# Optimization experiments

Measured on AMD Instinct MI355X. Metric: run time of the kernel, lower is better.

Reference implementation:

```python
import jax, jax.numpy as jnp
import numpy as np

N_NODES = 50000
N_EDGES = 800000
IN_F = 32
HID = 64
N_LAYERS = 3
BN_EPS = 1e-5


def setup_inputs() -> dict:
    key = jax.random.key(0)
    ks = jax.random.split(key, 8)
    x = jax.random.normal(ks[0], (N_NODES, IN_F), dtype=jnp.float32)
    edge_index = jax.random.randint(ks[1], (2, N_EDGES), 0, N_NODES, dtype=jnp.int64)
    W_embed = jax.random.normal(ks[2], (IN_F, HID), dtype=jnp.float32) / np.sqrt(IN_F)
    b_embed = jnp.zeros((HID,), dtype=jnp.float32)
    W_convs = jax.random.normal(ks[3], (N_LAYERS, HID, HID), dtype=jnp.float32) / np.sqrt(HID)
    b_convs = jnp.zeros((N_LAYERS, HID), dtype=jnp.float32)
    bn_gamma = jnp.ones((HID,), dtype=jnp.float32)
    bn_beta = jnp.zeros((HID,), dtype=jnp.float32)
    return {"x": x, "edge_index": edge_index, "W_embed": W_embed, "b_embed": b_embed,
            "W_convs": W_convs, "b_convs": b_convs, "bn_gamma": bn_gamma, "bn_beta": bn_beta}


def _gcn_norm(edge_index, n_nodes):
    # PyG GCNConv: add self-loops, symmetric normalization deg^-1/2 * deg^-1/2
    loops = jnp.arange(n_nodes, dtype=edge_index.dtype)
    src = jnp.concatenate([edge_index[0], loops])
    dst = jnp.concatenate([edge_index[1], loops])
    deg = jax.ops.segment_sum(jnp.ones_like(dst, dtype=jnp.float32), dst, num_segments=n_nodes)
    dinv = jax.lax.rsqrt(jnp.maximum(deg, 1.0))
    norm = dinv[src] * dinv[dst]  # [E+N]
    return src, dst, norm


def reference(x, edge_index, W_embed, b_embed, W_convs, b_convs, bn_gamma, bn_beta):
    n = x.shape[0]
    src, dst, norm = _gcn_norm(edge_index, n)

    h = jax.nn.relu(x @ W_embed + b_embed)  # [N, HID]
    for l in range(N_LAYERS):
        res = h
        # GCNConv: linear transform, then normalized neighbor aggregation
        t = h @ W_convs[l] + b_convs[l]
        msg = t[src] * norm[:, None]                           # [E+N, HID]
        agg = jax.ops.segment_sum(msg, dst, num_segments=n)    # [N, HID]
        # BatchNorm1d (training-mode batch stats), shared across layers
        mu = jnp.mean(agg, axis=0)
        var = jnp.var(agg, axis=0)
        bn = (agg - mu) * jax.lax.rsqrt(var + BN_EPS) * bn_gamma + bn_beta
        h = jax.nn.relu(bn) + res
    return h
```

## Files before the change

### kernel.cpp

```cpp
#include <hip/hip_runtime.h>

#define IN_F 32
#define HID 64
#define N_LAYERS 3
#define BN_EPS 1e-5f
#define NPLANE 4
#define PF 16

__device__ __forceinline__ unsigned short f2bf(float x) {
    unsigned u = __float_as_uint(x);
    u += 0x7fffu + ((u >> 16) & 1u);
    return (unsigned short)(u >> 16);
}
__device__ __forceinline__ float bflo(unsigned v) { return __uint_as_float(v << 16); }
__device__ __forceinline__ float bfhi(unsigned v) { return __uint_as_float(v & 0xffff0000u); }

__global__ __launch_bounds__(256) void k_zero(int* cnt, int* cursor, float* statsAll, int n) {
    int i = blockIdx.x * blockDim.x + threadIdx.x;
    if (i < n) cnt[i] = 0;
    if (i == 0) *cursor = 0;
    if (i < 2 * HID * N_LAYERS) statsAll[i] = 0.0f;
}

__global__ __launch_bounds__(256) void k_hist_rank(const int* __restrict__ dst, int* cnt,
                                                   unsigned short* __restrict__ rank, int e) {
    int i = blockIdx.x * blockDim.x + threadIdx.x;
    if (i >= e) return;
    int r = atomicAdd(&cnt[dst[i]], 1);
    rank[i] = (unsigned short)r;
}

__global__ __launch_bounds__(256) void k_assign(const int* __restrict__ cnt, int* rowbeg,
                                                float* dinv, int* cursor, int n) {
    int i = blockIdx.x * blockDim.x + threadIdx.x;
    int lane = threadIdx.x & 63;
    int c = (i < n) ? cnt[i] : 0;
    int s = c;
#pragma unroll
    for (int off = 1; off < 64; off <<= 1) {
        int t = __shfl_up(s, off, 64);
        if (lane >= off) s += t;
    }
    int total = __shfl(s, 63, 64);
    int base = 0;
    if (lane == 63) base = atomicAdd(cursor, total);
    base = __shfl(base, 63, 64);
    if (i < n) {
        rowbeg[i] = base + s - c;
        dinv[i] = rsqrtf((float)(c + 1));
    }
}

__global__ __launch_bounds__(256) void k_fill(const int* __restrict__ src,
                                              const int* __restrict__ dst,
                                              const int* __restrict__ rowbeg,
                                              const unsigned short* __restrict__ rank,
                                              unsigned short* __restrict__ csr_src, int e) {
    int i = blockIdx.x * blockDim.x + threadIdx.x;
    if (i >= e) return;
    int pos = rowbeg[dst[i]] + (int)rank[i];
    csr_src[pos] = (unsigned short)src[i];
}

__global__ __launch_bounds__(256, 4) void k_embed_conv(const float* __restrict__ x,
                                                       const float* __restrict__ We,
                                                       const float* __restrict__ be,
                                                       const float* __restrict__ Wc,
                                                       const float* __restrict__ bc,
                                                       const float* __restrict__ dinv,
                                                       float* __restrict__ h,
                                                       unsigned short* __restrict__ t2b, int n) {
    __shared__ float shx[4][IN_F];
    __shared__ float shh[4][HID];
    int f = threadIdx.x & 63;
    int wv = threadIdx.x >> 6;
    int plane = f >> 4, fin = f & 15;

    float we[IN_F];
#pragma unroll
    for (int k = 0; k < IN_F; ++k) we[k] = We[k * HID + f];
    float wc[HID];
#pragma unroll
    for (int k = 0; k < HID; ++k) wc[k] = Wc[k * HID + f];
    float bef = be[f], bcf = bc[f];

    int nw = gridDim.x * 4;
    for (int node = blockIdx.x * 4 + wv; node < n; node += nw) {
        if (f < IN_F) shx[wv][f] = x[(size_t)node * IN_F + f];
        float acc = bef;
#pragma unroll
        for (int k4 = 0; k4 < IN_F / 4; ++k4) {
            float4 xq = ((const float4*)shx[wv])[k4];
            acc = fmaf(xq.x, we[k4 * 4 + 0], acc);
            acc = fmaf(xq.y, we[k4 * 4 + 1], acc);
            acc = fmaf(xq.z, we[k4 * 4 + 2], acc);
            acc = fmaf(xq.w, we[k4 * 4 + 3], acc);
        }
        float hv = fmaxf(acc, 0.0f);
        h[(size_t)node * HID + f] = hv;
        shh[wv][f] = hv;
        float acc2 = bcf;
#pragma unroll
        for (int k4 = 0; k4 < HID / 4; ++k4) {
            float4 hq = ((const float4*)shh[wv])[k4];
            acc2 = fmaf(hq.x, wc[k4 * 4 + 0], acc2);
            acc2 = fmaf(hq.y, wc[k4 * 4 + 1], acc2);
            acc2 = fmaf(hq.z, wc[k4 * 4 + 2], acc2);
            acc2 = fmaf(hq.w, wc[k4 * 4 + 3], acc2);
        }
        t2b[(size_t)plane * n * PF + (size_t)node * PF + fin] = f2bf(acc2 * dinv[node]);
    }
}

__global__ __launch_bounds__(256, 4) void k_bn_conv(const float* __restrict__ agg,
                                                    const float* __restrict__ stats,
                                                    const float* __restrict__ gamma,
                                                    const float* __restrict__ beta,
                                                    const float* __restrict__ W,
                                                    const float* __restrict__ b,
                                                    const float* __restrict__ dinv,
                                                    float* __restrict__ h,
                                                    unsigned short* __restrict__ t2b, int n, float invN) {
    __shared__ float shh[4][HID];
    int f = threadIdx.x & 63;
    int wv = threadIdx.x >> 6;
    int plane = f >> 4, fin = f & 15;

    float wc[HID];
#pragma unroll
    for (int k = 0; k < HID; ++k) wc[k] = W[k * HID + f];

    float mu = stats[f] * invN;
    float var = fmaxf(stats[HID + f] * invN - mu * mu, 0.0f);
    float scale = rsqrtf(var + BN_EPS) * gamma[f];
    float shift = beta[f];
    float bf = b[f];

    int nw = gridDim.x * 4;
    for (int node = blockIdx.x * 4 + wv; node < n; node += nw) {
        size_t gid = (size_t)node * HID + f;
        float bnv = (agg[gid] - mu) * scale + shift;
        float hv = fmaxf(bnv, 0.0f) + h[gid];
        h[gid] = hv;
        shh[wv][f] = hv;
        float acc = bf;
#pragma unroll
        for (int k4 = 0; k4 < HID / 4; ++k4) {
            float4 hq = ((const float4*)shh[wv])[k4];
            acc = fmaf(hq.x, wc[k4 * 4 + 0], acc);
            acc = fmaf(hq.y, wc[k4 * 4 + 1], acc);
            acc = fmaf(hq.z, wc[k4 * 4 + 2], acc);
            acc = fmaf(hq.w, wc[k4 * 4 + 3], acc);
        }
        t2b[(size_t)plane * n * PF + (size_t)node * PF + fin] = f2bf(acc * dinv[node]);
    }
}

__global__ __launch_bounds__(256) void k_aggregate(const int* __restrict__ rowbeg,
                                                   const int* __restrict__ cnt,
                                                   const unsigned short* __restrict__ csr_src,
                                                   const unsigned short* __restrict__ t2b,
                                                   const float* __restrict__ dinv,
                                                   float* __restrict__ agg,
                                                   float* __restrict__ stats, int n) {
    __shared__ float lsum[PF], lsq[PF];
    if (threadIdx.x < PF) { lsum[threadIdx.x] = 0.0f; lsq[threadIdx.x] = 0.0f; }
    __syncthreads();

    const int plane = blockIdx.x & 3;
    const unsigned short* tb = t2b + (size_t)plane * n * PF;

    int l2 = threadIdx.x & 1;
    int node = (blockIdx.x >> 2) * 128 + (threadIdx.x >> 1);

    float4 r0 = make_float4(0.f, 0.f, 0.f, 0.f);
    float4 r1 = make_float4(0.f, 0.f, 0.f, 0.f);

    if (node < n) {
        int beg = rowbeg[node], end = beg + cnt[node];
        uint4 sv = ((const uint4*)(tb + (size_t)node * PF))[l2];
        float4 a0, a1;
        a0.x = bflo(sv.x); a0.y = bfhi(sv.x); a0.z = bflo(sv.y); a0.w = bfhi(sv.y);
        a1.x = bflo(sv.z); a1.y = bfhi(sv.z); a1.z = bflo(sv.w); a1.w = bfhi(sv.w);
        int j = beg;
        for (; j + 8 <= end; j += 8) {
            int s0 = csr_src[j + 0], s1 = csr_src[j + 1];
            int s2 = csr_src[j + 2], s3 = csr_src[j + 3];
            int s4 = csr_src[j + 4], s5 = csr_src[j + 5];
            int s6 = csr_src[j + 6], s7 = csr_src[j + 7];
            uint4 v0 = ((const uint4*)(tb + (size_t)s0 * PF))[l2];
            uint4 v1 = ((const uint4*)(tb + (size_t)s1 * PF))[l2];
            uint4 v2 = ((const uint4*)(tb + (size_t)s2 * PF))[l2];
            uint4 v3 = ((const uint4*)(tb + (size_t)s3 * PF))[l2];
            uint4 v4 = ((const uint4*)(tb + (size_t)s4 * PF))[l2];
            uint4 v5 = ((const uint4*)(tb + (size_t)s5 * PF))[l2];
            uint4 v6 = ((const uint4*)(tb + (size_t)s6 * PF))[l2];
            uint4 v7 = ((const uint4*)(tb + (size_t)s7 * PF))[l2];
            a0.x += bflo(v0.x) + bflo(v1.x) + bflo(v2.x) + bflo(v3.x)
                  + bflo(v4.x) + bflo(v5.x) + bflo(v6.x) + bflo(v7.x);
            a0.y += bfhi(v0.x) + bfhi(v1.x) + bfhi(v2.x) + bfhi(v3.x)
                  + bfhi(v4.x) + bfhi(v5.x) + bfhi(v6.x) + bfhi(v7.x);
            a0.z += bflo(v0.y) + bflo(v1.y) + bflo(v2.y) + bflo(v3.y)
                  + bflo(v4.y) + bflo(v5.y) + bflo(v6.y) + bflo(v7.y);
            a0.w += bfhi(v0.y) + bfhi(v1.y) + bfhi(v2.y) + bfhi(v3.y)
                  + bfhi(v4.y) + bfhi(v5.y) + bfhi(v6.y) + bfhi(v7.y);
            a1.x += bflo(v0.z) + bflo(v1.z) + bflo(v2.z) + bflo(v3.z)
                  + bflo(v4.z) + bflo(v5.z) + bflo(v6.z) + bflo(v7.z);
            a1.y += bfhi(v0.z) + bfhi(v1.z) + bfhi(v2.z) + bfhi(v3.z)
                  + bfhi(v4.z) + bfhi(v5.z) + bfhi(v6.z) + bfhi(v7.z);
            a1.z += bflo(v0.w) + bflo(v1.w) + bflo(v2.w) + bflo(v3.w)
                  + bflo(v4.w) + bflo(v5.w) + bflo(v6.w) + bflo(v7.w);
            a1.w += bfhi(v0.w) + bfhi(v1.w) + bfhi(v2.w) + bfhi(v3.w)
                  + bfhi(v4.w) + bfhi(v5.w) + bfhi(v6.w) + bfhi(v7.w);
        }
        for (; j < end; ++j) {
            int s = csr_src[j];
            uint4 v = ((const uint4*)(tb + (size_t)s * PF))[l2];
            a0.x += bflo(v.x); a0.y += bfhi(v.x); a0.z += bflo(v.y); a0.w += bfhi(v.y);
            a1.x += bflo(v.z); a1.y += bfhi(v.z); a1.z += bflo(v.w); a1.w += bfhi(v.w);
        }
        float dv = dinv[node];
        r0.x = a0.x * dv; r0.y = a0.y * dv; r0.z = a0.z * dv; r0.w = a0.w * dv;
        r1.x = a1.x * dv; r1.y = a1.y * dv; r1.z = a1.z * dv; r1.w = a1.w * dv;
        float4* ar = (float4*)(agg + (size_t)node * HID + plane * PF + l2 * 8);
        ar[0] = r0;
        ar[1] = r1;
    }

    float4 q0, q1;
    q0.x = r0.x * r0.x; q0.y = r0.y * r0.y; q0.z = r0.z * r0.z; q0.w = r0.w * r0.w;
    q1.x = r1.x * r1.x; q1.y = r1.y * r1.y; q1.z = r1.z * r1.z; q1.w = r1.w * r1.w;
#pragma unroll
    for (int off = 2; off < 64; off <<= 1) {
        r0.x += __shfl_xor(r0.x, off, 64); q0.x += __shfl_xor(q0.x, off, 64);
        r0.y += __shfl_xor(r0.y, off, 64); q0.y += __shfl_xor(q0.y, off, 64);
        r0.z += __shfl_xor(r0.z, off, 64); q0.z += __shfl_xor(q0.z, off, 64);
        r0.w += __shfl_xor(r0.w, off, 64); q0.w += __shfl_xor(q0.w, off, 64);
        r1.x += __shfl_xor(r1.x, off, 64); q1.x += __shfl_xor(q1.x, off, 64);
        r1.y += __shfl_xor(r1.y, off, 64); q1.y += __shfl_xor(q1.y, off, 64);
        r1.z += __shfl_xor(r1.z, off, 64); q1.z += __shfl_xor(q1.z, off, 64);
        r1.w += __shfl_xor(r1.w, off, 64); q1.w += __shfl_xor(q1.w, off, 64);
    }
    if ((threadIdx.x & 63) < 2) {
        int f0 = l2 * 8;
        atomicAdd(&lsum[f0 + 0], r0.x); atomicAdd(&lsq[f0 + 0], q0.x);
        atomicAdd(&lsum[f0 + 1], r0.y); atomicAdd(&lsq[f0 + 1], q0.y);
        atomicAdd(&lsum[f0 + 2], r0.z); atomicAdd(&lsq[f0 + 2], q0.z);
        atomicAdd(&lsum[f0 + 3], r0.w); atomicAdd(&lsq[f0 + 3], q0.w);
        atomicAdd(&lsum[f0 + 4], r1.x); atomicAdd(&lsq[f0 + 4], q1.x);
        atomicAdd(&lsum[f0 + 5], r1.y); atomicAdd(&lsq[f0 + 5], q1.y);
        atomicAdd(&lsum[f0 + 6], r1.z); atomicAdd(&lsq[f0 + 6], q1.z);
        atomicAdd(&lsum[f0 + 7], r1.w); atomicAdd(&lsq[f0 + 7], q1.w);
    }
    __syncthreads();
    if (threadIdx.x < PF) {
        atomicAdd(&stats[plane * PF + threadIdx.x], lsum[threadIdx.x]);
        atomicAdd(&stats[HID + plane * PF + threadIdx.x], lsq[threadIdx.x]);
    }
}

__global__ __launch_bounds__(256) void k_bn_apply(const float* __restrict__ agg,
                                                  const float* __restrict__ stats,
                                                  const float* __restrict__ gamma,
                                                  const float* __restrict__ beta,
                                                  float* __restrict__ h, int n, float invN) {
    int gid = blockIdx.x * blockDim.x + threadIdx.x;
    int node = gid >> 6, f = gid & 63;
    if (node >= n) return;
    float mu = stats[f] * invN;
    float var = fmaxf(stats[HID + f] * invN - mu * mu, 0.0f);
    float bn = (agg[gid] - mu) * rsqrtf(var + BN_EPS) * gamma[f] + beta[f];
    h[gid] = fmaxf(bn, 0.0f) + h[gid];
}

extern "C" void kernel_launch(void* const* d_in, const int* in_sizes, int n_in,
                              void* d_out, int out_size, void* d_ws, size_t ws_size,
                              hipStream_t stream) {
    const float* x       = (const float*)d_in[0];
    const int*   ei      = (const int*)d_in[1];
    const float* W_embed = (const float*)d_in[2];
    const float* b_embed = (const float*)d_in[3];
    const float* W_convs = (const float*)d_in[4];
    const float* b_convs = (const float*)d_in[5];
    const float* gamma   = (const float*)d_in[6];
    const float* beta    = (const float*)d_in[7];
    float* h = (float*)d_out;

    const int n = in_sizes[0] / IN_F;
    const int e = in_sizes[1] / 2;
    const int* src = ei;
    const int* dst = ei + e;

    unsigned short* t2b = (unsigned short*)d_ws;
    float* agg      = (float*)(t2b + (size_t)n * HID);
    float* dinv     = agg + (size_t)n * HID;
    float* statsAll = dinv + n;
    int*   rowbeg   = (int*)(statsAll + 2 * HID * N_LAYERS);
    int*   cnt      = rowbeg + n;
    int*   cursor   = cnt + n;
    unsigned short* csr_src = (unsigned short*)(cursor + 1);
    unsigned short* rank    = csr_src + e;

    const int nodeBlocks  = (n + 255) / 256;
    const int nfBlocks    = (n * HID + 255) / 256;
    const int edgeBlocks  = (e + 255) / 256;
    const int aggBlocks   = ((n + 127) / 128) * NPLANE;
    const int denseBlocks = 1024;

    k_zero<<<nodeBlocks, 256, 0, stream>>>(cnt, cursor, statsAll, n);
    k_hist_rank<<<edgeBlocks, 256, 0, stream>>>(dst, cnt, rank, e);
    k_assign<<<nodeBlocks, 256, 0, stream>>>(cnt, rowbeg, dinv, cursor, n);
    k_fill<<<edgeBlocks, 256, 0, stream>>>(src, dst, rowbeg, rank, csr_src, e);

    const float invN = 1.0f / (float)n;

    k_embed_conv<<<denseBlocks, 256, 0, stream>>>(x, W_embed, b_embed, W_convs, b_convs,
                                                  dinv, h, t2b, n);

    for (int l = 0; l < N_LAYERS; ++l) {
        float* stats = statsAll + (size_t)l * 2 * HID;
        k_aggregate<<<aggBlocks, 256, 0, stream>>>(rowbeg, cnt, csr_src, t2b, dinv,
                                                   agg, stats, n);
        if (l < N_LAYERS - 1) {
            const float* Wl = W_convs + (size_t)(l + 1) * HID * HID;
            const float* bl = b_convs + (size_t)(l + 1) * HID;
            k_bn_conv<<<denseBlocks, 256, 0, stream>>>(agg, stats, gamma, beta, Wl, bl, dinv,
                                                       h, t2b, n, invN);
        } else {
            k_bn_apply<<<nfBlocks, 256, 0, stream>>>(agg, stats, gamma, beta, h, n, invN);
        }
    }
}
```

Baseline: 218.4 us.

## Fuse CSR fill with embedding kernel, memset zeroing, nontemporal streaming accesses

Merges the CSR fill kernel and the embed+first-conv kernel into one launch, with block ranges split by role so the two independent stages can run concurrently. The zeroing kernel becomes a single hipMemsetAsync, which requires moving the stats buffer to sit contiguously after cnt and cursor. Streamed buffers (rank, csr_src, agg) now use nontemporal loads and stores to reduce cache pollution. The fused kernel uses the embed kernel's launch bounds for the fill blocks too, and the nontemporal hints may hurt if the data would otherwise have been reused from cache.

```diff
diff --git a/kernel.cpp b/kernel.cpp
--- a/kernel.cpp
+++ b/kernel.cpp
@@ -7,6 +7,8 @@
 #define NPLANE 4
 #define PF 16
 
+typedef float f32x4 __attribute__((ext_vector_type(4)));
+
 __device__ __forceinline__ unsigned short f2bf(float x) {
     unsigned u = __float_as_uint(x);
     u += 0x7fffu + ((u >> 16) & 1u);
@@ -14,20 +16,13 @@
 }
 __device__ __forceinline__ float bflo(unsigned v) { return __uint_as_float(v << 16); }
 __device__ __forceinline__ float bfhi(unsigned v) { return __uint_as_float(v & 0xffff0000u); }
-
-__global__ __launch_bounds__(256) void k_zero(int* cnt, int* cursor, float* statsAll, int n) {
-    int i = blockIdx.x * blockDim.x + threadIdx.x;
-    if (i < n) cnt[i] = 0;
-    if (i == 0) *cursor = 0;
-    if (i < 2 * HID * N_LAYERS) statsAll[i] = 0.0f;
-}
 
 __global__ __launch_bounds__(256) void k_hist_rank(const int* __restrict__ dst, int* cnt,
                                                    unsigned short* __restrict__ rank, int e) {
     int i = blockIdx.x * blockDim.x + threadIdx.x;
     if (i >= e) return;
     int r = atomicAdd(&cnt[dst[i]], 1);
-    rank[i] = (unsigned short)r;
+    __builtin_nontemporal_store((unsigned short)r, &rank[i]);
 }
 
 __global__ __launch_bounds__(256) void k_assign(const int* __restrict__ cnt, int* rowbeg,
@@ -51,27 +46,34 @@
     }
 }
 
-__global__ __launch_bounds__(256) void k_fill(const int* __restrict__ src,
-                                              const int* __restrict__ dst,
-                                              const int* __restrict__ rowbeg,
-                                              const unsigned short* __restrict__ rank,
-                                              unsigned short* __restrict__ csr_src, int e) {
-    int i = blockIdx.x * blockDim.x + threadIdx.x;
-    if (i >= e) return;
-    int pos = rowbeg[dst[i]] + (int)rank[i];
-    csr_src[pos] = (unsigned short)src[i];
-}
-
-__global__ __launch_bounds__(256, 4) void k_embed_conv(const float* __restrict__ x,
+__global__ __launch_bounds__(256, 4) void k_fill_embed(const int* __restrict__ src,
+                                                       const int* __restrict__ dst,
+                                                       const int* __restrict__ rowbeg,
+                                                       const unsigned short* __restrict__ rank,
+                                                       unsigned short* __restrict__ csr_src, int e,
+                                                       int fillBlocks,
+                                                       const float* __restrict__ x,
                                                        const float* __restrict__ We,
                                                        const float* __restrict__ be,
                                                        const float* __restrict__ Wc,
                                                        const float* __restrict__ bc,
                                                        const float* __restrict__ dinv,
                                                        float* __restrict__ h,
-                                                       unsigned short* __restrict__ t2b, int n) {
+                                                       unsigned short* __restrict__ t2b, int n,
+                                                       int denseBlocks) {
     __shared__ float shx[4][IN_F];
     __shared__ float shh[4][HID];
+
+    if (blockIdx.x < fillBlocks) {
+        int i = blockIdx.x * blockDim.x + threadIdx.x;
+        if (i < e) {
+            int pos = rowbeg[dst[i]] + (int)__builtin_nontemporal_load(&rank[i]);
+            __builtin_nontemporal_store((unsigned short)src[i], &csr_src[pos]);
+        }
+        return;
+    }
+
+    int bid = blockIdx.x - fillBlocks;
     int f = threadIdx.x & 63;
     int wv = threadIdx.x >> 6;
     int plane = f >> 4, fin = f & 15;
@@ -84,8 +86,8 @@
     for (int k = 0; k < HID; ++k) wc[k] = Wc[k * HID + f];
     float bef = be[f], bcf = bc[f];
 
-    int nw = gridDim.x * 4;
-    for (int node = blockIdx.x * 4 + wv; node < n; node += nw) {
+    int nw = denseBlocks * 4;
+    for (int node = bid * 4 + wv; node < n; node += nw) {
         if (f < IN_F) shx[wv][f] = x[(size_t)node * IN_F + f];
         float acc = bef;
 #pragma unroll
@@ -139,7 +141,8 @@
     int nw = gridDim.x * 4;
     for (int node = blockIdx.x * 4 + wv; node < n; node += nw) {
         size_t gid = (size_t)node * HID + f;
-        float bnv = (agg[gid] - mu) * scale + shift;
+        float av = __builtin_nontemporal_load(&agg[gid]);
+        float bnv = (av - mu) * scale + shift;
         float hv = fmaxf(bnv, 0.0f) + h[gid];
         h[gid] = hv;
         shh[wv][f] = hv;
@@ -184,10 +187,14 @@
         a1.x = bflo(sv.z); a1.y = bfhi(sv.z); a1.z = bflo(sv.w); a1.w = bfhi(sv.w);
         int j = beg;
         for (; j + 8 <= end; j += 8) {
-            int s0 = csr_src[j + 0], s1 = csr_src[j + 1];
-            int s2 = csr_src[j + 2], s3 = csr_src[j + 3];
-            int s4 = csr_src[j + 4], s5 = csr_src[j + 5];
-            int s6 = csr_src[j + 6], s7 = csr_src[j + 7];
+            int s0 = __builtin_nontemporal_load(&csr_src[j + 0]);
+            int s1 = __builtin_nontemporal_load(&csr_src[j + 1]);
+            int s2 = __builtin_nontemporal_load(&csr_src[j + 2]);
+            int s3 = __builtin_nontemporal_load(&csr_src[j + 3]);
+            int s4 = __builtin_nontemporal_load(&csr_src[j + 4]);
+            int s5 = __builtin_nontemporal_load(&csr_src[j + 5]);
+            int s6 = __builtin_nontemporal_load(&csr_src[j + 6]);
+            int s7 = __builtin_nontemporal_load(&csr_src[j + 7]);
             uint4 v0 = ((const uint4*)(tb + (size_t)s0 * PF))[l2];
             uint4 v1 = ((const uint4*)(tb + (size_t)s1 * PF))[l2];
             uint4 v2 = ((const uint4*)(tb + (size_t)s2 * PF))[l2];
@@ -214,7 +221,7 @@
                   + bfhi(v4.w) + bfhi(v5.w) + bfhi(v6.w) + bfhi(v7.w);
         }
         for (; j < end; ++j) {
-            int s = csr_src[j];
+            int s = __builtin_nontemporal_load(&csr_src[j]);
             uint4 v = ((const uint4*)(tb + (size_t)s * PF))[l2];
             a0.x += bflo(v.x); a0.y += bfhi(v.x); a0.z += bflo(v.y); a0.w += bfhi(v.y);
             a1.x += bflo(v.z); a1.y += bfhi(v.z); a1.z += bflo(v.w); a1.w += bfhi(v.w);
@@ -222,9 +229,11 @@
         float dv = dinv[node];
         r0.x = a0.x * dv; r0.y = a0.y * dv; r0.z = a0.z * dv; r0.w = a0.w * dv;
         r1.x = a1.x * dv; r1.y = a1.y * dv; r1.z = a1.z * dv; r1.w = a1.w * dv;
-        float4* ar = (float4*)(agg + (size_t)node * HID + plane * PF + l2 * 8);
-        ar[0] = r0;
-        ar[1] = r1;
+        f32x4* ar = (f32x4*)(agg + (size_t)node * HID + plane * PF + l2 * 8);
+        f32x4 n0 = { r0.x, r0.y, r0.z, r0.w };
+        f32x4 n1 = { r1.x, r1.y, r1.z, r1.w };
+        __builtin_nontemporal_store(n0, &ar[0]);
+        __builtin_nontemporal_store(n1, &ar[1]);
     }
 
     float4 q0, q1;
@@ -269,7 +278,8 @@
     if (node >= n) return;
     float mu = stats[f] * invN;
     float var = fmaxf(stats[HID + f] * invN - mu * mu, 0.0f);
-    float bn = (agg[gid] - mu) * rsqrtf(var + BN_EPS) * gamma[f] + beta[f];
+    float av = __builtin_nontemporal_load(&agg[gid]);
+    float bn = (av - mu) * rsqrtf(var + BN_EPS) * gamma[f] + beta[f];
     h[gid] = fmaxf(bn, 0.0f) + h[gid];
 }
 
@@ -294,11 +304,11 @@
     unsigned short* t2b = (unsigned short*)d_ws;
     float* agg      = (float*)(t2b + (size_t)n * HID);
     float* dinv     = agg + (size_t)n * HID;
-    float* statsAll = dinv + n;
-    int*   rowbeg   = (int*)(statsAll + 2 * HID * N_LAYERS);
+    int*   rowbeg   = (int*)(dinv + n);
     int*   cnt      = rowbeg + n;
     int*   cursor   = cnt + n;
-    unsigned short* csr_src = (unsigned short*)(cursor + 1);
+    float* statsAll = (float*)(cursor + 1);
+    unsigned short* csr_src = (unsigned short*)(statsAll + 2 * HID * N_LAYERS);
     unsigned short* rank    = csr_src + e;
 
     const int nodeBlocks  = (n + 255) / 256;
@@ -307,15 +317,16 @@
     const int aggBlocks   = ((n + 127) / 128) * NPLANE;
     const int denseBlocks = 1024;
 
-    k_zero<<<nodeBlocks, 256, 0, stream>>>(cnt, cursor, statsAll, n);
+    (void)hipMemsetAsync(cnt, 0, (size_t)(n + 1 + 2 * HID * N_LAYERS) * sizeof(int), stream);
+
     k_hist_rank<<<edgeBlocks, 256, 0, stream>>>(dst, cnt, rank, e);
     k_assign<<<nodeBlocks, 256, 0, stream>>>(cnt, rowbeg, dinv, cursor, n);
-    k_fill<<<edgeBlocks, 256, 0, stream>>>(src, dst, rowbeg, rank, csr_src, e);
 
     const float invN = 1.0f / (float)n;
 
-    k_embed_conv<<<denseBlocks, 256, 0, stream>>>(x, W_embed, b_embed, W_convs, b_convs,
-                                                  dinv, h, t2b, n);
+    k_fill_embed<<<edgeBlocks + denseBlocks, 256, 0, stream>>>(
+        src, dst, rowbeg, rank, csr_src, e, edgeBlocks,
+        x, W_embed, b_embed, W_convs, b_convs, dinv, h, t2b, n, denseBlocks);
 
     for (int l = 0; l < N_LAYERS; ++l) {
         float* stats = statsAll + (size_t)l * 2 * HID;
```

Result: slower. 269.8 us (+23.5%).
